# Performance work log

Measured on AMD Instinct MI355X. Metric: run time of the kernel, lower is better.

The kernel has to match this reference:

```python
import jax, jax.numpy as jnp
import numpy as np

IN_DIM = 128
HID = 128
NUM_CLASSES = 10
N_NODES = 100000
N_EDGES = 1600000
NUM_GRAPHS = 128


def setup_inputs() -> dict:
    key = jax.random.key(0)
    ks = jax.random.split(key, 12)
    X = jax.random.normal(ks[0], (N_NODES, IN_DIM), dtype=jnp.float32)
    EI = jax.random.randint(ks[1], (2, N_EDGES), 0, N_NODES, dtype=jnp.int64)
    batch = jnp.sort(jax.random.randint(ks[2], (N_NODES,), 0, NUM_GRAPHS, dtype=jnp.int64))
    s_in = 1.0 / np.sqrt(IN_DIM)
    s_h = 1.0 / np.sqrt(HID)
    s_m = 1.0 / np.sqrt(2 * HID)
    params = {
        'W1': jax.random.uniform(ks[3], (IN_DIM, HID), jnp.float32, -s_in, s_in),
        'b1': jnp.zeros((HID,), jnp.float32),
        'W2': jax.random.uniform(ks[4], (HID, HID), jnp.float32, -s_h, s_h),
        'b2': jnp.zeros((HID,), jnp.float32),
        'W3': jax.random.uniform(ks[5], (HID, HID), jnp.float32, -s_h, s_h),
        'b3': jnp.zeros((HID,), jnp.float32),
        'Wm1': jax.random.uniform(ks[6], (2 * HID, HID), jnp.float32, -s_m, s_m),
        'bm1': jnp.zeros((HID,), jnp.float32),
        'Wm2': jax.random.uniform(ks[7], (HID, NUM_CLASSES), jnp.float32, -s_h, s_h),
        'bm2': jnp.zeros((NUM_CLASSES,), jnp.float32),
    }
    return dict(X=X, EI=EI, batch=batch, num_graphs=NUM_GRAPHS, **params)


def _gcn_norm(EI, n):
    # add self loops, compute D^{-1/2}[row] * D^{-1/2}[col]
    loops = jnp.arange(n, dtype=EI.dtype)
    row = jnp.concatenate([EI[0], loops])
    col = jnp.concatenate([EI[1], loops])
    deg = jax.ops.segment_sum(jnp.ones_like(row, dtype=jnp.float32), row, num_segments=n)
    dis = (deg + 1e-12) ** -0.5
    norm = dis[row] * dis[col]
    return row, col, norm


def _gcn_layer(x, row, col, norm, W, b):
    h = x @ W + b                       # [N, out]
    msg = h[col] * norm[:, None]        # gather + scale  [E+N, out]
    return jax.ops.segment_sum(msg, row, num_segments=x.shape[0])  # scatter-add


def _pool_mean_max(x, batch, num_graphs):
    s = jax.ops.segment_sum(x, batch, num_segments=num_graphs)
    cnt = jax.ops.segment_sum(jnp.ones((x.shape[0],), x.dtype), batch, num_segments=num_graphs)
    mean = s / (cnt[:, None] + 1e-12)
    mx = jax.ops.segment_max(x, batch, num_segments=num_graphs)
    return jnp.concatenate([mean, mx], axis=1)


def reference(X, EI, batch, num_graphs, W1, b1, W2, b2, W3, b3, Wm1, bm1, Wm2, bm2):
    n = X.shape[0]
    row, col, norm = _gcn_norm(EI, n)
    x = jax.nn.relu(_gcn_layer(X, row, col, norm, W1, b1))
    x = jax.nn.relu(_gcn_layer(x, row, col, norm, W2, b2))
    x = jax.nn.relu(_gcn_layer(x, row, col, norm, W3, b3))
    g = _pool_mean_max(x, batch, num_graphs)
    h = jax.nn.relu(g @ Wm1 + bm1)
    return h @ Wm2 + bm2
```

## Files before the change

### kernel.cpp

```cpp
#include <hip/hip_runtime.h>
#include <hip/hip_fp16.h>
#include <cstdint>
#include <cstddef>

#define DIM 128
#define NG 128
#define NCLS 10
#define PSLICE 8
#define CPAD 64
#define NXCD 8
#define BCHUNK 4096
#define XCCID_IMM ((31 << 11) | (0 << 6) | 20)

typedef _Float16 f16;
typedef __attribute__((ext_vector_type(8))) _Float16 f16x8;
typedef __attribute__((ext_vector_type(4))) float f32x4;


__global__ __launch_bounds__(256) void k_build(
    const int* __restrict__ rw, const int* __restrict__ cl, int E, int N,
    int* __restrict__ cnt, int* __restrict__ csrc, int* __restrict__ work) {
  __shared__ int sbase;
  unsigned xcc = __builtin_amdgcn_s_getreg(XCCID_IMM) & (NXCD - 1);
  int lo = (int)((long long)N * xcc / NXCD);
  int hi = (int)((long long)N * (xcc + 1) / NXCD);
  for (;;) {
    if (threadIdx.x == 0) sbase = atomicAdd(&work[xcc], BCHUNK);
    __syncthreads();
    int b = sbase;
    __syncthreads();
    if (b >= E) break;
    int e = b + BCHUNK;
    if (e > E) e = E;
    for (int i = b + (int)threadIdx.x; i < e; i += 256) {
      int r = __builtin_nontemporal_load(rw + i);
      if (r >= lo && r < hi) {
        int c = __builtin_nontemporal_load(cl + i);
        int sl = atomicAdd(&cnt[r], 1);
        if (sl < CPAD) csrc[((size_t)r << 6) + sl] = c;
      }
    }
  }
}

__global__ void k_dis(const int* __restrict__ cnt, float* __restrict__ dis, int N) {
  int i = blockIdx.x * blockDim.x + threadIdx.x;
  if (i < N) {
    float d = (float)(cnt[i] + 1);
    dis[i] = 1.0f / sqrtf(d);
  }
}

__global__ void k_wt(const float* __restrict__ W, __half* __restrict__ Wt) {
  int i = blockIdx.x * 256 + threadIdx.x;
  if (i >= DIM * DIM) return;
  int k = i >> 7, c = i & 127;
  Wt[(size_t)c * DIM + k] = __float2half(W[(size_t)k * DIM + c]);
}


template <int FP32IN>
__global__ __launch_bounds__(256, 3) void k_gemm(
    const void* __restrict__ Ain, const __half* __restrict__ Wt,
    const float* __restrict__ bias, const float* __restrict__ dis,
    __half* __restrict__ Hh, int N) {
  int t = threadIdx.x;
  int lane = t & 63;
  int wv = t >> 6;
  int l15 = lane & 15, lg = lane >> 4;
  int cb = (wv & 1) * 64;

  f16x8 bfr[4][4];
#pragma unroll
  for (int ct = 0; ct < 4; ++ct) {
    int c = cb + ct * 16 + l15;
    const f16* wp = (const f16*)Wt + (size_t)c * DIM + lg * 8;
#pragma unroll
    for (int ks = 0; ks < 4; ++ks) bfr[ks][ct] = *(const f16x8*)(wp + ks * 32);
  }
  float bv[4];
#pragma unroll
  for (int ct = 0; ct < 4; ++ct) bv[ct] = bias[cb + ct * 16 + l15];

  const int nt2 = (N + 31) / 32;
  for (int t2 = blockIdx.x; t2 < nt2; t2 += gridDim.x) {
    int row0 = t2 * 32 + (wv >> 1) * 16;
    int rA = row0 + l15;
    if (rA > N - 1) rA = N - 1;
    f16x8 afr[4];
    if constexpr (FP32IN) {
      const float* ap = (const float*)Ain + (size_t)rA * DIM + lg * 8;
#pragma unroll
      for (int ks = 0; ks < 4; ++ks) {
        float4 v0 = *(const float4*)(ap + ks * 32);
        float4 v1 = *(const float4*)(ap + ks * 32 + 4);
        f16x8 a;
        a[0] = (f16)v0.x; a[1] = (f16)v0.y; a[2] = (f16)v0.z; a[3] = (f16)v0.w;
        a[4] = (f16)v1.x; a[5] = (f16)v1.y; a[6] = (f16)v1.z; a[7] = (f16)v1.w;
        afr[ks] = a;
      }
    } else {
      const f16* ap = (const f16*)Ain + (size_t)rA * DIM + lg * 8;
#pragma unroll
      for (int ks = 0; ks < 4; ++ks) afr[ks] = *(const f16x8*)(ap + ks * 32);
    }

    f32x4 acc[4];
#pragma unroll
    for (int ct = 0; ct < 4; ++ct) acc[ct] = (f32x4){0.f, 0.f, 0.f, 0.f};
#pragma unroll
    for (int ks = 0; ks < 4; ++ks)
#pragma unroll
      for (int ct = 0; ct < 4; ++ct)
        acc[ct] = __builtin_amdgcn_mfma_f32_16x16x32_f16(afr[ks], bfr[ks][ct], acc[ct], 0, 0, 0);

#pragma unroll
    for (int j = 0; j < 4; ++j) {
      int r = row0 + lg * 4 + j;
      if (r < N) {
        float dr = dis[r];
#pragma unroll
        for (int ct = 0; ct < 4; ++ct) {
          float o = (acc[ct][j] + bv[ct]) * dr;
          Hh[(size_t)r * DIM + cb + ct * 16 + l15] = __float2half(o);
        }
      }
    }
  }
}


__global__ __launch_bounds__(256) void k_agg(
    const __half* __restrict__ Hh, __half* __restrict__ Ah,
    const int* __restrict__ csrc, const int* __restrict__ cntA,
    const float* __restrict__ dis, int N) {
  int wid = (int)(((size_t)blockIdx.x * blockDim.x + threadIdx.x) >> 6);
  int lane = threadIdx.x & 63;
  if (wid >= N) return;
  int half = lane >> 5;
  int q = lane & 31;
  int cnt = cntA[wid];
  if (cnt > CPAD) cnt = CPAD;
  float dr = dis[wid];
  const int* cp = csrc + ((size_t)wid << 6);
  float4 a0 = {0.f, 0.f, 0.f, 0.f};
  float4 a1 = {0.f, 0.f, 0.f, 0.f};
  float4 a2 = {0.f, 0.f, 0.f, 0.f};
  float4 a3 = {0.f, 0.f, 0.f, 0.f};
  int i = half;
  for (; i + 6 < cnt; i += 8) {
    int c0 = cp[i], c1 = cp[i + 2], c2 = cp[i + 4], c3 = cp[i + 6];
    uint2 u0 = *(const uint2*)(Hh + (size_t)c0 * DIM + q * 4);
    uint2 u1 = *(const uint2*)(Hh + (size_t)c1 * DIM + q * 4);
    uint2 u2 = *(const uint2*)(Hh + (size_t)c2 * DIM + q * 4);
    uint2 u3 = *(const uint2*)(Hh + (size_t)c3 * DIM + q * 4);
    float2 f;
    f = __half22float2(*reinterpret_cast<__half2*>(&u0.x)); a0.x += f.x; a0.y += f.y;
    f = __half22float2(*reinterpret_cast<__half2*>(&u0.y)); a0.z += f.x; a0.w += f.y;
    f = __half22float2(*reinterpret_cast<__half2*>(&u1.x)); a1.x += f.x; a1.y += f.y;
    f = __half22float2(*reinterpret_cast<__half2*>(&u1.y)); a1.z += f.x; a1.w += f.y;
    f = __half22float2(*reinterpret_cast<__half2*>(&u2.x)); a2.x += f.x; a2.y += f.y;
    f = __half22float2(*reinterpret_cast<__half2*>(&u2.y)); a2.z += f.x; a2.w += f.y;
    f = __half22float2(*reinterpret_cast<__half2*>(&u3.x)); a3.x += f.x; a3.y += f.y;
    f = __half22float2(*reinterpret_cast<__half2*>(&u3.y)); a3.z += f.x; a3.w += f.y;
  }
  for (; i < cnt; i += 2) {
    int c0 = cp[i];
    uint2 u0 = *(const uint2*)(Hh + (size_t)c0 * DIM + q * 4);
    float2 f;
    f = __half22float2(*reinterpret_cast<__half2*>(&u0.x)); a0.x += f.x; a0.y += f.y;
    f = __half22float2(*reinterpret_cast<__half2*>(&u0.y)); a0.z += f.x; a0.w += f.y;
  }
  float ax = (a0.x + a1.x) + (a2.x + a3.x);
  float ay = (a0.y + a1.y) + (a2.y + a3.y);
  float az = (a0.z + a1.z) + (a2.z + a3.z);
  float aw = (a0.w + a1.w) + (a2.w + a3.w);
  ax += __shfl_xor(ax, 32);
  ay += __shfl_xor(ay, 32);
  az += __shfl_xor(az, 32);
  aw += __shfl_xor(aw, 32);
  if (lane < 32) {
    uint2 us = *(const uint2*)(Hh + (size_t)wid * DIM + q * 4);
    float2 s0 = __half22float2(*reinterpret_cast<__half2*>(&us.x));
    float2 s1 = __half22float2(*reinterpret_cast<__half2*>(&us.y));
    float ox = fmaxf(dr * (ax + s0.x), 0.f);
    float oy = fmaxf(dr * (ay + s0.y), 0.f);
    float oz = fmaxf(dr * (az + s1.x), 0.f);
    float ow = fmaxf(dr * (aw + s1.y), 0.f);
    __half2 p0 = __floats2half2_rn(ox, oy);
    __half2 p1 = __floats2half2_rn(oz, ow);
    uint2 u;
    u.x = *(unsigned int*)&p0;
    u.y = *(unsigned int*)&p1;
    *(uint2*)(Ah + (size_t)wid * DIM + q * 4) = u;
  }
}


__global__ void k_bounds(const int* __restrict__ batch, int N, int G,
                         int* __restrict__ starts) {
  int i = blockIdx.x * blockDim.x + threadIdx.x;
  if (i >= N) return;
  int b = batch[i];
  int pb = (i == 0) ? -1 : batch[i - 1];
  for (int g = pb + 1; g <= b; ++g) starts[g] = i;
  if (i == N - 1) {
    for (int g = b + 1; g <= G; ++g) starts[g] = N;
  }
}

__global__ void k_pool1(const __half* __restrict__ A, const int* __restrict__ starts,
                        float* __restrict__ part) {
  int g = blockIdx.x / PSLICE, sl = blockIdx.x % PSLICE;
  int c = threadIdx.x;
  int s = starts[g], e = starts[g + 1];
  int len = e - s;
  int ns = s + (len * sl) / PSLICE;
  int ne = s + (len * (sl + 1)) / PSLICE;
  float sum = 0.f, mx = -INFINITY;
  for (int n = ns; n < ne; ++n) {
    float v = __half2float(A[(size_t)n * DIM + c]);
    sum += v;
    mx = fmaxf(mx, v);
  }
  part[((size_t)(g * PSLICE + sl) * 2 + 0) * DIM + c] = sum;
  part[((size_t)(g * PSLICE + sl) * 2 + 1) * DIM + c] = mx;
}

__global__ void k_pool2(const float* __restrict__ part, const int* __restrict__ starts,
                        float* __restrict__ GF) {
  int g = blockIdx.x;
  int c = threadIdx.x;
  float sum = 0.f, mx = -INFINITY;
  for (int sl = 0; sl < PSLICE; ++sl) {
    sum += part[((size_t)(g * PSLICE + sl) * 2 + 0) * DIM + c];
    mx = fmaxf(mx, part[((size_t)(g * PSLICE + sl) * 2 + 1) * DIM + c]);
  }
  int cntg = starts[g + 1] - starts[g];
  GF[(size_t)g * 256 + c] = sum / ((float)cntg + 1e-12f);
  GF[(size_t)g * 256 + 128 + c] = mx;
}


__global__ void k_mlp1(const float* __restrict__ GF, const float* __restrict__ Wm1,
                       const float* __restrict__ bm1, float* __restrict__ H1) {
  __shared__ float gs[256];
  int g = blockIdx.x, j = threadIdx.x;
  gs[j] = GF[(size_t)g * 256 + j];
  gs[j + 128] = GF[(size_t)g * 256 + 128 + j];
  __syncthreads();
  float acc = bm1[j];
#pragma unroll 8
  for (int k = 0; k < 256; ++k) acc = fmaf(gs[k], Wm1[k * DIM + j], acc);
  H1[(size_t)g * DIM + j] = fmaxf(acc, 0.f);
}

__global__ void k_mlp2(const float* __restrict__ H1, const float* __restrict__ Wm2,
                       const float* __restrict__ bm2, float* __restrict__ out) {
  __shared__ float hs[DIM];
  int g = blockIdx.x, j = threadIdx.x;
  hs[j] = H1[(size_t)g * DIM + j];
  hs[j + 64] = H1[(size_t)g * DIM + j + 64];
  __syncthreads();
  if (j < NCLS) {
    float acc = bm2[j];
#pragma unroll 8
    for (int k = 0; k < DIM; ++k) acc = fmaf(hs[k], Wm2[k * NCLS + j], acc);
    out[(size_t)g * NCLS + j] = acc;
  }
}


static inline size_t al256(size_t x) { return (x + 255) & ~(size_t)255; }

extern "C" void kernel_launch(void* const* d_in, const int* in_sizes, int n_in,
                              void* d_out, int out_size, void* d_ws, size_t ws_size,
                              hipStream_t stream) {
  const float* X = (const float*)d_in[0];
  const int* EI = (const int*)d_in[1];
  const int* batch = (const int*)d_in[2];
  const float* W1 = (const float*)d_in[4];
  const float* b1 = (const float*)d_in[5];
  const float* W2 = (const float*)d_in[6];
  const float* b2 = (const float*)d_in[7];
  const float* W3 = (const float*)d_in[8];
  const float* b3 = (const float*)d_in[9];
  const float* Wm1 = (const float*)d_in[10];
  const float* bm1 = (const float*)d_in[11];
  const float* Wm2 = (const float*)d_in[12];
  const float* bm2 = (const float*)d_in[13];
  float* OUT = (float*)d_out;

  const int N = in_sizes[0] / DIM;
  const int E = in_sizes[1] / 2;
  const int G = NG;

  const int* EI_row = EI;
  const int* EI_col = EI + E;

  char* p = (char*)d_ws;
  size_t off = 0;
  auto take = [&](size_t bytes) { void* r = p + off; off = al256(off + bytes); return r; };

  int* cnt = (int*)take((size_t)N * 4);
  int* work = (int*)take((size_t)NXCD * 4);
  int* starts = (int*)take((size_t)(G + 1) * 4);
  float* dis = (float*)take((size_t)N * 4);
  int* csrc = (int*)take((size_t)N * CPAD * 4);
  __half* Hh = (__half*)take((size_t)N * DIM * 2);
  __half* Ah = (__half*)take((size_t)N * DIM * 2);
  __half* Wt1 = (__half*)take((size_t)DIM * DIM * 2);
  __half* Wt2 = (__half*)take((size_t)DIM * DIM * 2);
  __half* Wt3 = (__half*)take((size_t)DIM * DIM * 2);
  float* part = (float*)take((size_t)G * PSLICE * 2 * DIM * 4);
  float* GF = (float*)take((size_t)G * 256 * 4);
  float* H1 = (float*)take((size_t)G * DIM * 4);
  (void)ws_size; (void)n_in; (void)out_size;

  hipMemsetAsync(cnt, 0, (size_t)N * 4, stream);
  hipMemsetAsync(work, 0, (size_t)NXCD * 4, stream);

  k_build<<<1024, 256, 0, stream>>>(EI_row, EI_col, E, N, cnt, csrc, work);
  k_dis<<<(N + 255) / 256, 256, 0, stream>>>(cnt, dis, N);
  k_wt<<<64, 256, 0, stream>>>(W1, Wt1);
  k_wt<<<64, 256, 0, stream>>>(W2, Wt2);
  k_wt<<<64, 256, 0, stream>>>(W3, Wt3);

  const int aggBlocks = (int)(((size_t)N * 64 + 255) / 256);

  k_gemm<1><<<512, 256, 0, stream>>>(X, Wt1, b1, dis, Hh, N);
  k_agg<<<aggBlocks, 256, 0, stream>>>(Hh, Ah, csrc, cnt, dis, N);
  k_gemm<0><<<512, 256, 0, stream>>>(Ah, Wt2, b2, dis, Hh, N);
  k_agg<<<aggBlocks, 256, 0, stream>>>(Hh, Ah, csrc, cnt, dis, N);
  k_gemm<0><<<512, 256, 0, stream>>>(Ah, Wt3, b3, dis, Hh, N);
  k_agg<<<aggBlocks, 256, 0, stream>>>(Hh, Ah, csrc, cnt, dis, N);

  k_bounds<<<(N + 255) / 256, 256, 0, stream>>>(batch, N, G, starts);
  k_pool1<<<G * PSLICE, DIM, 0, stream>>>(Ah, starts, part);
  k_pool2<<<G, DIM, 0, stream>>>(part, starts, GF);

  k_mlp1<<<G, DIM, 0, stream>>>(GF, Wm1, bm1, H1);
  k_mlp2<<<G, 64, 0, stream>>>(H1, Wm2, bm2, OUT);
}
```

Measured before the change: 457.7 us.

## Partition edges into per-XCD buckets before building padded CSR

Replaces the single CSR build pass, in which every XCD scanned all edges and filtered by row range, with two passes. The first buckets edges by destination XCD into per-block fixed-capacity slots as packed 64-bit pairs. The second has each XCD consume only its own buckets, so the full edge list is read once instead of once per XCD. It also merges the three weight-transpose launches into one. In exchange it adds an extra launch and buffer traffic, and any bucket over PCAP=384 entries silently drops edges; the expected fill is 1600000/(1024*8) ≈ 195, so random inputs stay under the cap.

```diff
diff --git a/kernel.cpp b/kernel.cpp
--- a/kernel.cpp
+++ b/kernel.cpp
@@ -9,7 +9,8 @@
 #define PSLICE 8
 #define CPAD 64
 #define NXCD 8
-#define BCHUNK 4096
+#define NPBLK 1024
+#define PCAP 384
 #define XCCID_IMM ((31 << 11) | (0 << 6) | 20)
 
 typedef _Float16 f16;
@@ -17,28 +18,51 @@
 typedef __attribute__((ext_vector_type(4))) float f32x4;
 
 
-__global__ __launch_bounds__(256) void k_build(
+__global__ __launch_bounds__(256) void k_part(
     const int* __restrict__ rw, const int* __restrict__ cl, int E, int N,
+    unsigned long long* __restrict__ buckets, int* __restrict__ bcnt) {
+  __shared__ int lcnt[NXCD];
+  if (threadIdx.x < NXCD) lcnt[threadIdx.x] = 0;
+  __syncthreads();
+  int b = blockIdx.x;
+  int C = (E + NPBLK - 1) / NPBLK;
+  int s = b * C;
+  int e = s + C;
+  if (e > E) e = E;
+  for (int i = s + (int)threadIdx.x; i < e; i += 256) {
+    int r = rw[i], c = cl[i];
+    int o = (int)(((long long)r * NXCD) / N);
+    int sl = atomicAdd(&lcnt[o], 1);
+    if (sl < PCAP)
+      buckets[((size_t)o * NPBLK + b) * PCAP + sl] =
+          ((unsigned long long)(unsigned)r << 32) | (unsigned)c;
+  }
+  __syncthreads();
+  if (threadIdx.x < NXCD) {
+    int v = lcnt[threadIdx.x];
+    bcnt[threadIdx.x * NPBLK + b] = v < PCAP ? v : PCAP;
+  }
+}
+
+__global__ __launch_bounds__(256) void k_place(
+    const unsigned long long* __restrict__ buckets, const int* __restrict__ bcnt,
     int* __restrict__ cnt, int* __restrict__ csrc, int* __restrict__ work) {
-  __shared__ int sbase;
+  __shared__ int sseg;
   unsigned xcc = __builtin_amdgcn_s_getreg(XCCID_IMM) & (NXCD - 1);
-  int lo = (int)((long long)N * xcc / NXCD);
-  int hi = (int)((long long)N * (xcc + 1) / NXCD);
   for (;;) {
-    if (threadIdx.x == 0) sbase = atomicAdd(&work[xcc], BCHUNK);
+    if (threadIdx.x == 0) sseg = atomicAdd(&work[xcc], 1);
     __syncthreads();
-    int b = sbase;
+    int seg = sseg;
     __syncthreads();
-    if (b >= E) break;
-    int e = b + BCHUNK;
-    if (e > E) e = E;
-    for (int i = b + (int)threadIdx.x; i < e; i += 256) {
-      int r = __builtin_nontemporal_load(rw + i);
-      if (r >= lo && r < hi) {
-        int c = __builtin_nontemporal_load(cl + i);
-        int sl = atomicAdd(&cnt[r], 1);
-        if (sl < CPAD) csrc[((size_t)r << 6) + sl] = c;
-      }
+    if (seg >= NPBLK) break;
+    int n = bcnt[xcc * NPBLK + seg];
+    const unsigned long long* bp = buckets + ((size_t)xcc * NPBLK + seg) * PCAP;
+    for (int j = (int)threadIdx.x; j < n; j += 256) {
+      unsigned long long ent = bp[j];
+      int r = (int)(unsigned)(ent >> 32);
+      int c = (int)(unsigned)(ent & 0xffffffffu);
+      int sl = atomicAdd(&cnt[r], 1);
+      if (sl < CPAD) csrc[(r << 6) + sl] = c;
     }
   }
 }
@@ -51,9 +75,14 @@
   }
 }
 
-__global__ void k_wt(const float* __restrict__ W, __half* __restrict__ Wt) {
-  int i = blockIdx.x * 256 + threadIdx.x;
-  if (i >= DIM * DIM) return;
+__global__ void k_wt(const float* __restrict__ W1, const float* __restrict__ W2,
+                     const float* __restrict__ W3, __half* __restrict__ Wt1,
+                     __half* __restrict__ Wt2, __half* __restrict__ Wt3) {
+  int gi = blockIdx.x * 256 + threadIdx.x;
+  int m = gi / (DIM * DIM);
+  int i = gi % (DIM * DIM);
+  const float* W = (m == 0) ? W1 : (m == 1) ? W2 : W3;
+  __half* Wt = (m == 0) ? Wt1 : (m == 1) ? Wt2 : Wt3;
   int k = i >> 7, c = i & 127;
   Wt[(size_t)c * DIM + k] = __float2half(W[(size_t)k * DIM + c]);
 }
@@ -304,9 +333,12 @@
 
   int* cnt = (int*)take((size_t)N * 4);
   int* work = (int*)take((size_t)NXCD * 4);
+  int* bcnt = (int*)take((size_t)NXCD * NPBLK * 4);
   int* starts = (int*)take((size_t)(G + 1) * 4);
   float* dis = (float*)take((size_t)N * 4);
   int* csrc = (int*)take((size_t)N * CPAD * 4);
+  unsigned long long* buckets =
+      (unsigned long long*)take((size_t)NXCD * NPBLK * PCAP * 8);
   __half* Hh = (__half*)take((size_t)N * DIM * 2);
   __half* Ah = (__half*)take((size_t)N * DIM * 2);
   __half* Wt1 = (__half*)take((size_t)DIM * DIM * 2);
@@ -320,11 +352,10 @@
   hipMemsetAsync(cnt, 0, (size_t)N * 4, stream);
   hipMemsetAsync(work, 0, (size_t)NXCD * 4, stream);
 
-  k_build<<<1024, 256, 0, stream>>>(EI_row, EI_col, E, N, cnt, csrc, work);
+  k_part<<<NPBLK, 256, 0, stream>>>(EI_row, EI_col, E, N, buckets, bcnt);
+  k_place<<<1024, 256, 0, stream>>>(buckets, bcnt, cnt, csrc, work);
   k_dis<<<(N + 255) / 256, 256, 0, stream>>>(cnt, dis, N);
-  k_wt<<<64, 256, 0, stream>>>(W1, Wt1);
-  k_wt<<<64, 256, 0, stream>>>(W2, Wt2);
-  k_wt<<<64, 256, 0, stream>>>(W3, Wt3);
+  k_wt<<<192, 256, 0, stream>>>(W1, W2, W3, Wt1, Wt2, Wt3);
 
   const int aggBlocks = (int)(((size_t)N * 64 + 255) / 256);
 
```

Result: no change. 459.9 us (+0.5%).
